# Performance work log

Measured on AMD Instinct MI355X. Metric: run time of the kernel, lower is better.

The kernel has to match this reference:

```python
import jax, jax.numpy as jnp
import numpy as np

N_NODES = 100000
N_EDGES = 1600000
IN_FEATS = 128
OUT_FEATS = 32
NEG_SLOPE = 0.2


def setup_inputs() -> dict:
    key = jax.random.key(0)
    k1, k2, k3, k4, k5 = jax.random.split(key, 5)
    h = jax.random.normal(k1, (N_NODES, IN_FEATS), dtype=jnp.float32)
    W = jax.random.normal(k2, (OUT_FEATS, IN_FEATS), dtype=jnp.float32) * 0.1
    a = jax.random.normal(k3, (1, 2 * OUT_FEATS), dtype=jnp.float32) * 0.1
    src = jax.random.randint(k4, (N_EDGES,), 0, N_NODES)
    dst = jax.random.randint(k5, (N_EDGES,), 0, N_NODES)
    return {"h": h, "W": W, "a": a, "src": src, "dst": dst}


def reference(h, W, a, src, dst):
    # feat dropout is identity in eval mode (feat_drop=0)
    z = h @ W.T                                   # [N, D] node projections
    # attention_func([z_src || z_dst]) = z_src @ a_l + z_dst @ a_r (no bias)
    a_l, a_r = a[0, :OUT_FEATS], a[0, OUT_FEATS:]
    el = z @ a_l                                  # [N]
    er = z @ a_r                                  # [N]
    e = jax.nn.leaky_relu(el[src] + er[dst], NEG_SLOPE)   # [E]
    # segment softmax over incoming edges per destination node
    e_max = jax.ops.segment_max(e, dst, num_segments=N_NODES)      # [N]
    e_max = jnp.where(jnp.isfinite(e_max), e_max, 0.0)             # empty segments
    ex = jnp.exp(e - e_max[dst])                                   # [E]
    denom = jax.ops.segment_sum(ex, dst, num_segments=N_NODES)     # [N]
    alpha = ex / jnp.maximum(denom[dst], 1e-16)                    # [E]
    # attn dropout identity in eval mode; weighted scatter-sum of messages
    msg = alpha[:, None] * z[src]                                  # [E, D]
    out = jax.ops.segment_sum(msg, dst, num_segments=N_NODES)      # [N, D]
    return out
```

## Files before the change

kernel.cpp:

```cpp
#include <hip/hip_runtime.h>
#include <hip/hip_bf16.h>

#define N_NODES_C  100000
#define N_EDGES_C  1600000
#define IN_FEATS_C 128
#define OUT_FEATS_C 32
#define NEG_SLOPE_C 0.2f
#define NCH 8

typedef __attribute__((ext_vector_type(8))) short short8;
typedef __attribute__((ext_vector_type(4))) float f32x4;

__device__ __hip_bfloat16 g_zb[N_NODES_C * OUT_FEATS_C];
__device__ float  g_el[N_NODES_C];
__device__ float  g_er[N_NODES_C];
__device__ int    g_head[NCH][N_NODES_C];
__device__ int2   g_ns[N_EDGES_C];
__device__ short8 g_wf_hi[2][4][64];
__device__ short8 g_wf_lo[2][4][64];

static __device__ __forceinline__ unsigned short f2bf(float x) {
    unsigned int u = __float_as_uint(x);
    unsigned int r = (u + 0x7FFFu + ((u >> 16) & 1u)) >> 16;
    return (unsigned short)r;
}
static __device__ __forceinline__ float bf2f(unsigned short h) {
    return __uint_as_float(((unsigned int)h) << 16);
}

__global__ __launch_bounds__(256) void k_prep(const float* __restrict__ W, int nheads, int nbn)
{
    int b = blockIdx.x;
    if (b < nbn) {
        int i = b * 256 + threadIdx.x;
        if (i < nheads) ((int*)g_head)[i] = -1;
        return;
    }
    int i = (b - nbn) * 256 + threadIdx.x;
    if (i >= 512) return;
    int lane = i & 63;
    int kt   = (i >> 6) & 3;
    int nt   = i >> 8;
    int row  = nt * 16 + (lane & 15);
    const float* p = W + (size_t)row * IN_FEATS_C + kt * 32 + (lane >> 4) * 8;
    float4 x0 = *(const float4*)(p);
    float4 x1 = *(const float4*)(p + 4);
    float xs[8] = {x0.x, x0.y, x0.z, x0.w, x1.x, x1.y, x1.z, x1.w};
    short8 hi, lo;
#pragma unroll
    for (int j = 0; j < 8; ++j) {
        unsigned short hb = f2bf(xs[j]);
        hi[j] = (short)hb;
        lo[j] = (short)f2bf(xs[j] - bf2f(hb));
    }
    g_wf_hi[nt][kt][lane] = hi;
    g_wf_lo[nt][kt][lane] = lo;
}

__global__ __launch_bounds__(256) void k_fat(const float* __restrict__ h,
                                             const float* __restrict__ a,
                                             const int* __restrict__ src,
                                             const int* __restrict__ dst,
                                             int n_nodes, int n_edges,
                                             int PB, int LB)
{
    int bid = blockIdx.x;
    if (bid % 5 == 0) {
        int pidx = bid / 5;
        if (pidx >= PB) return;
        int tile = pidx * 4 + (threadIdx.x >> 6);
        int ntiles = (n_nodes + 15) / 16;
        if (tile >= ntiles) return;
        int l   = threadIdx.x & 63;
        int r16 = l & 15;
        int g   = l >> 4;

        const float* hrow = h + (size_t)(tile * 16 + r16) * IN_FEATS_C + g * 8;
        f32x4 acc0 = {0.f, 0.f, 0.f, 0.f};
        f32x4 acc1 = {0.f, 0.f, 0.f, 0.f};

#pragma unroll
        for (int kt = 0; kt < 4; ++kt) {
            float4 x0 = *(const float4*)(hrow + kt * 32);
            float4 x1 = *(const float4*)(hrow + kt * 32 + 4);
            float xs[8] = {x0.x, x0.y, x0.z, x0.w, x1.x, x1.y, x1.z, x1.w};
            short8 ahi, alo;
#pragma unroll
            for (int j = 0; j < 8; ++j) {
                unsigned short hb = f2bf(xs[j]);
                ahi[j] = (short)hb;
                alo[j] = (short)f2bf(xs[j] - bf2f(hb));
            }
            short8 bh0 = g_wf_hi[0][kt][l], bl0 = g_wf_lo[0][kt][l];
            short8 bh1 = g_wf_hi[1][kt][l], bl1 = g_wf_lo[1][kt][l];
            acc0 = __builtin_amdgcn_mfma_f32_16x16x32_bf16(ahi, bh0, acc0, 0, 0, 0);
            acc0 = __builtin_amdgcn_mfma_f32_16x16x32_bf16(alo, bh0, acc0, 0, 0, 0);
            acc0 = __builtin_amdgcn_mfma_f32_16x16x32_bf16(ahi, bl0, acc0, 0, 0, 0);
            acc1 = __builtin_amdgcn_mfma_f32_16x16x32_bf16(ahi, bh1, acc1, 0, 0, 0);
            acc1 = __builtin_amdgcn_mfma_f32_16x16x32_bf16(alo, bh1, acc1, 0, 0, 0);
            acc1 = __builtin_amdgcn_mfma_f32_16x16x32_bf16(ahi, bl1, acc1, 0, 0, 0);
        }

        float al0 = a[r16], al1 = a[16 + r16];
        float ar0 = a[32 + r16], ar1 = a[48 + r16];
        float elp[4], erp[4];
        unsigned short* zb = (unsigned short*)g_zb;
#pragma unroll
        for (int r = 0; r < 4; ++r) {
            float z0 = acc0[r], z1 = acc1[r];
            int node = tile * 16 + g * 4 + r;
            zb[(size_t)node * OUT_FEATS_C + r16]      = f2bf(z0);
            zb[(size_t)node * OUT_FEATS_C + 16 + r16] = f2bf(z1);
            elp[r] = z0 * al0 + z1 * al1;
            erp[r] = z0 * ar0 + z1 * ar1;
        }
#pragma unroll
        for (int m = 1; m <= 8; m <<= 1) {
#pragma unroll
            for (int r = 0; r < 4; ++r) {
                elp[r] += __shfl_xor(elp[r], m, 64);
                erp[r] += __shfl_xor(erp[r], m, 64);
            }
        }
        int nodeb = tile * 16 + g * 4;
        if (r16 == 0) {
#pragma unroll
            for (int r = 0; r < 4; ++r) g_el[nodeb + r] = elp[r];
        } else if (r16 == 1) {
#pragma unroll
            for (int r = 0; r < 4; ++r) g_er[nodeb + r] = erp[r];
        }
    } else {
        int lidx = 4 * (bid / 5) + (bid % 5) - 1;
        if (lidx >= LB) return;
        int e = lidx * 256 + threadIdx.x;
        if (e < n_edges) {
            int nxt = atomicExch(&g_head[e & (NCH - 1)][dst[e]], e);
            g_ns[e] = make_int2(nxt, src[e]);
        }
    }
}

__global__ __launch_bounds__(256) void k_gather(float* __restrict__ out, int n_nodes)
{
    int tid  = blockIdx.x * blockDim.x + threadIdx.x;
    int node = tid >> 6;
    if (node >= n_nodes) return;
    int l = threadIdx.x & 63;
    int c = l >> 3;
    int q = l & 7;

    float er_d = g_er[node];
    const unsigned short* zb = (const unsigned short*)g_zb;
    float a0 = 0.f, a1 = 0.f, a2 = 0.f, a3 = 0.f, den = 0.f;

    int j = g_head[c][node];
    int2 ns = make_int2(-1, 0);
    if (j >= 0) ns = g_ns[j];
    while (j >= 0) {
        int jn = ns.x;
        int s  = ns.y;
        int2 ns2 = make_int2(-1, 0);
        if (jn >= 0) ns2 = g_ns[jn];
        float x = g_el[s] + er_d;
        x = (x > 0.f) ? x : NEG_SLOPE_C * x;
        float ex = __expf(x);
        ushort4 zv = *(const ushort4*)(zb + (size_t)s * OUT_FEATS_C + q * 4);
        a0 = fmaf(ex, bf2f(zv.x), a0);
        a1 = fmaf(ex, bf2f(zv.y), a1);
        a2 = fmaf(ex, bf2f(zv.z), a2);
        a3 = fmaf(ex, bf2f(zv.w), a3);
        den += ex;
        j = jn;
        ns = ns2;
    }
#pragma unroll
    for (int m = 8; m <= 32; m <<= 1) {
        a0  += __shfl_xor(a0,  m, 64);
        a1  += __shfl_xor(a1,  m, 64);
        a2  += __shfl_xor(a2,  m, 64);
        a3  += __shfl_xor(a3,  m, 64);
        den += __shfl_xor(den, m, 64);
    }
    if (c == 0) {
        float inv = 1.0f / fmaxf(den, 1e-16f);
        float4 o = make_float4(a0 * inv, a1 * inv, a2 * inv, a3 * inv);
        ((float4*)(out + (size_t)node * OUT_FEATS_C))[q] = o;
    }
}

extern "C" void kernel_launch(void* const* d_in, const int* in_sizes, int n_in,
                              void* d_out, int out_size, void* d_ws, size_t ws_size,
                              hipStream_t stream) {
    const float* h   = (const float*)d_in[0];
    const float* W   = (const float*)d_in[1];
    const float* a   = (const float*)d_in[2];
    const int*   src = (const int*)d_in[3];
    const int*   dst = (const int*)d_in[4];
    float* out = (float*)d_out;

    const int n_nodes = in_sizes[0] / IN_FEATS_C;
    const int n_edges = in_sizes[3];

    const int nheads = NCH * n_nodes;
    const int nbn    = (nheads + 255) / 256;
    const int ntiles = (n_nodes + 15) / 16;
    const int PB     = (ntiles + 3) / 4;
    const int LB     = (n_edges + 255) / 256;
    const int G      = 5 * ((PB > (LB + 3) / 4) ? PB : (LB + 3) / 4);

    k_prep<<<nbn + 2, 256, 0, stream>>>(W, nheads, nbn);
    k_fat<<<G, 256, 0, stream>>>(h, a, src, dst, n_nodes, n_edges, PB, LB);
    k_gather<<<(n_nodes * 64 + 255) / 256, 256, 0, stream>>>(out, n_nodes);
}
```

Measured before the change: 140.9 us.

## Use 16 edge chains per node with node-major heads and 16-byte feature loads

Doubles the number of per-destination linked-list chains from 8 to 16, so each chain is about half as long and the dependent pointer-chasing latency in the gather shrinks. The head array becomes node-major so a node's 16 heads sit contiguously. Each lane now loads 8 bf16 features with one 16-byte load instead of 4, and the cross-lane reduction gains one extra shuffle stage. The init kernel clears twice as many head entries, and each lane keeps more accumulator registers live.

```diff
diff --git a/kernel.cpp b/kernel.cpp
--- a/kernel.cpp
+++ b/kernel.cpp
@@ -6,7 +6,7 @@
 #define IN_FEATS_C 128
 #define OUT_FEATS_C 32
 #define NEG_SLOPE_C 0.2f
-#define NCH 8
+#define NCH 16
 
 typedef __attribute__((ext_vector_type(8))) short short8;
 typedef __attribute__((ext_vector_type(4))) float f32x4;
@@ -14,7 +14,7 @@
 __device__ __hip_bfloat16 g_zb[N_NODES_C * OUT_FEATS_C];
 __device__ float  g_el[N_NODES_C];
 __device__ float  g_er[N_NODES_C];
-__device__ int    g_head[NCH][N_NODES_C];
+__device__ int    g_head[N_NODES_C][NCH];
 __device__ int2   g_ns[N_EDGES_C];
 __device__ short8 g_wf_hi[2][4][64];
 __device__ short8 g_wf_lo[2][4][64];
@@ -135,7 +135,7 @@
         if (lidx >= LB) return;
         int e = lidx * 256 + threadIdx.x;
         if (e < n_edges) {
-            int nxt = atomicExch(&g_head[e & (NCH - 1)][dst[e]], e);
+            int nxt = atomicExch(&g_head[dst[e]][e & (NCH - 1)], e);
             g_ns[e] = make_int2(nxt, src[e]);
         }
     }
@@ -147,14 +147,15 @@
     int node = tid >> 6;
     if (node >= n_nodes) return;
     int l = threadIdx.x & 63;
-    int c = l >> 3;
-    int q = l & 7;
+    int c = l >> 2;
+    int q = l & 3;
 
     float er_d = g_er[node];
     const unsigned short* zb = (const unsigned short*)g_zb;
-    float a0 = 0.f, a1 = 0.f, a2 = 0.f, a3 = 0.f, den = 0.f;
-
-    int j = g_head[c][node];
+    float a0 = 0.f, a1 = 0.f, a2 = 0.f, a3 = 0.f;
+    float a4 = 0.f, a5 = 0.f, a6 = 0.f, a7 = 0.f, den = 0.f;
+
+    int j = g_head[node][c];
     int2 ns = make_int2(-1, 0);
     if (j >= 0) ns = g_ns[j];
     while (j >= 0) {
@@ -165,27 +166,36 @@
         float x = g_el[s] + er_d;
         x = (x > 0.f) ? x : NEG_SLOPE_C * x;
         float ex = __expf(x);
-        ushort4 zv = *(const ushort4*)(zb + (size_t)s * OUT_FEATS_C + q * 4);
-        a0 = fmaf(ex, bf2f(zv.x), a0);
-        a1 = fmaf(ex, bf2f(zv.y), a1);
-        a2 = fmaf(ex, bf2f(zv.z), a2);
-        a3 = fmaf(ex, bf2f(zv.w), a3);
+        short8 zv = *(const short8*)(zb + (size_t)s * OUT_FEATS_C + q * 8);
+        a0 = fmaf(ex, bf2f((unsigned short)zv[0]), a0);
+        a1 = fmaf(ex, bf2f((unsigned short)zv[1]), a1);
+        a2 = fmaf(ex, bf2f((unsigned short)zv[2]), a2);
+        a3 = fmaf(ex, bf2f((unsigned short)zv[3]), a3);
+        a4 = fmaf(ex, bf2f((unsigned short)zv[4]), a4);
+        a5 = fmaf(ex, bf2f((unsigned short)zv[5]), a5);
+        a6 = fmaf(ex, bf2f((unsigned short)zv[6]), a6);
+        a7 = fmaf(ex, bf2f((unsigned short)zv[7]), a7);
         den += ex;
         j = jn;
         ns = ns2;
     }
 #pragma unroll
-    for (int m = 8; m <= 32; m <<= 1) {
+    for (int m = 4; m <= 32; m <<= 1) {
         a0  += __shfl_xor(a0,  m, 64);
         a1  += __shfl_xor(a1,  m, 64);
         a2  += __shfl_xor(a2,  m, 64);
         a3  += __shfl_xor(a3,  m, 64);
+        a4  += __shfl_xor(a4,  m, 64);
+        a5  += __shfl_xor(a5,  m, 64);
+        a6  += __shfl_xor(a6,  m, 64);
+        a7  += __shfl_xor(a7,  m, 64);
         den += __shfl_xor(den, m, 64);
     }
     if (c == 0) {
         float inv = 1.0f / fmaxf(den, 1e-16f);
-        float4 o = make_float4(a0 * inv, a1 * inv, a2 * inv, a3 * inv);
-        ((float4*)(out + (size_t)node * OUT_FEATS_C))[q] = o;
+        float* orow = out + (size_t)node * OUT_FEATS_C + q * 8;
+        *(float4*)(orow)     = make_float4(a0 * inv, a1 * inv, a2 * inv, a3 * inv);
+        *(float4*)(orow + 4) = make_float4(a4 * inv, a5 * inv, a6 * inv, a7 * inv);
     }
 }
 
```

Result: no change. 138.4 us (-1.8%).
